# Optimization experiments

Hardware: AMD Instinct MI355X
Metric: run time of the kernel (lower is better)

The kernel has to match this reference:

```python
import jax, jax.numpy as jnp
import numpy as np


def setup_inputs() -> dict:
    key = jax.random.key(0)
    B, D, C, H = 4096, 64, 128, 512
    ks = jax.random.split(key, 6)
    return {
        "q_z_x_params": jax.random.normal(ks[0], (B, C), jnp.float32),
        "eps": jax.random.normal(ks[1], (B, D), jnp.float32),
        "W1": jax.random.normal(ks[2], (D + C, H), jnp.float32) / np.sqrt(D + C).astype(np.float32),
        "b1": jnp.zeros((H,), jnp.float32),
        "W2": jax.random.normal(ks[3], (H, H), jnp.float32) / np.sqrt(H).astype(np.float32),
        "b2": jnp.zeros((H,), jnp.float32),
        "W3": jax.random.normal(ks[4], (H, 2 * D), jnp.float32) / np.sqrt(H).astype(np.float32),
        "b3": jnp.zeros((2 * D,), jnp.float32),
    }


def _made_masks(D, C, H):
    # Standard MADE degrees, natural ordering; context columns fully connected.
    m_in = np.arange(1, D + 1)                      # input degrees 1..D
    m_h = (np.arange(H) % (D - 1)) + 1              # hidden degrees 1..D-1
    M1 = np.concatenate([m_h[None, :] >= m_in[:, None],
                         np.ones((C, H), bool)], axis=0)   # (D+C, H)
    M2 = m_h[None, :] >= m_h[:, None]               # (H, H)
    m_out = np.tile(np.arange(1, D + 1), 2)         # (2D,) mean||prescale
    M3 = m_out[None, :] > m_h[:, None]              # (H, 2D)
    f32 = jnp.float32
    return jnp.asarray(M1, f32), jnp.asarray(M2, f32), jnp.asarray(M3, f32)


def reference(q_z_x_params, eps, W1, b1, W2, b2, W3, b3):
    B, D = eps.shape
    C = q_z_x_params.shape[1]
    H = W2.shape[0]
    M1, M2, M3 = _made_masks(D, C, H)
    mW1, mW2, mW3 = W1 * M1, W2 * M2, W3 * M3

    def made(z):
        x = jnp.concatenate([z, q_z_x_params], axis=1)   # (B, D+C)
        h1 = jax.nn.relu(x @ mW1 + b1)
        h2 = jax.nn.relu(h1 @ mW2 + b2)
        out = h2 @ mW3 + b3                              # (B, 2D)
        return out[:, :D], out[:, D:]

    def step(z, i):
        mean, prescale = made(z)
        mu_i = jnp.take(mean, i, axis=1)                 # (B,)
        scale_i = jax.nn.softplus(jnp.take(prescale, i, axis=1))
        z_i = mu_i + scale_i * jnp.take(eps, i, axis=1)  # reparameterized Normal sample
        z = z.at[:, i].set(z_i)
        return z, None

    z0 = jnp.zeros((B, D), eps.dtype)
    z_sample, _ = jax.lax.scan(step, z0, jnp.arange(D))
    return z_sample
```

## Files before the change

kernel.cpp:

```cpp
#include <hip/hip_runtime.h>
#include <math.h>

#define DD 64
#define CC 128
#define HH 512
#define BATCH 4096

typedef __attribute__((ext_vector_type(2))) float f32x2;
typedef unsigned long long u64;

__device__ __forceinline__ f32x2 splat2(float x) { f32x2 v; v[0] = x; v[1] = x; return v; }

__device__ __forceinline__ f32x2 pk_fma(f32x2 a, f32x2 b, f32x2 c) {
    f32x2 d;
    asm("v_pk_fma_f32 %0, %1, %2, %3" : "=v"(d) : "v"(a), "v"(b), "v"(c));
    return d;
}
__device__ __forceinline__ f32x2 pk_fma_s(u64 hpair, f32x2 b, f32x2 c) {
    f32x2 d;
    asm("v_pk_fma_f32 %0, %1, %2, %3" : "=v"(d) : "s"(hpair), "v"(b), "v"(c));
    return d;
}

__device__ __forceinline__ float fast_softplus(float x) {
    float t = exp2f(-fabsf(x) * 1.44269504f);
    return fmaxf(x, 0.f) + 0.69314718f * log2f(1.f + t);
}

__device__ __forceinline__ float bcast(float x, int l) {
    return __int_as_float(__builtin_amdgcn_readlane(__float_as_int(x), l));
}
__device__ __forceinline__ u64 rl_pair(float x, int l) {
    unsigned u = (unsigned)__builtin_amdgcn_readlane(__float_as_int(x), l);
    return ((u64)u << 32) | u;
}

typedef const __attribute__((address_space(1))) void* as1_cptr;
typedef __attribute__((address_space(3))) void* as3_ptr;
__device__ __forceinline__ void glds16(const float* g, float* l) {
    __builtin_amdgcn_global_load_lds((as1_cptr)g, (as3_ptr)l, 16, 0, 0);
}

__global__ __launch_bounds__(512, 2) void made_sample(
    const float* __restrict__ ctx,
    const float* __restrict__ eps,
    const float* __restrict__ W1,
    const float* __restrict__ b1,
    const float* __restrict__ W2,
    const float* __restrict__ b2,
    const float* __restrict__ W3,
    const float* __restrict__ b3,
    float* __restrict__ out)
{
    const int lane  = threadIdx.x & 63;
    const int w     = threadIdx.x >> 6;
    const int rbase = blockIdx.x * 16 + w * 2;
    const int jbase = 8 * lane;

    __shared__ float sbuf[2][10 * HH];
    __shared__ float w3sb[2][5 * 256];

    int deg[8];
    #pragma unroll
    for (int u = 0; u < 8; ++u) deg[u] = (jbase + u) % 63 + 1;

    auto load8v = [&](const float* base_, f32x2* r_) {
        float4 a = *(const float4*)(base_ + lane * 4);
        float4 b = *(const float4*)(base_ + 256 + lane * 4);
        r_[0][0] = a.x; r_[0][1] = a.y; r_[1][0] = a.z; r_[1][1] = a.w;
        r_[2][0] = b.x; r_[2][1] = b.y; r_[3][0] = b.z; r_[3][1] = b.w;
    };
    auto stage_row = [&](const float* src, float* dst) {
        glds16(src + lane * 8,     dst);
        glds16(src + lane * 8 + 4, dst + 256);
    };
    auto stage_w3pair = [&](int k0, int k1, float* dst) {
        const float* g = (lane < 32) ? (W3 + k0 * (2 * DD) + lane * 4)
                                     : (W3 + k1 * (2 * DD) + (lane - 32) * 4);
        glds16(g, dst);
    };

    f32x2 p1[2][4], p2[2][4], acc[2];
    #pragma unroll
    for (int j = 0; j < 4; ++j) {
        f32x2 t1, t2;
        t1[0] = b1[jbase + 2 * j]; t1[1] = b1[jbase + 2 * j + 1];
        t2[0] = b2[jbase + 2 * j]; t2[1] = b2[jbase + 2 * j + 1];
        p1[0][j] = t1; p1[1][j] = t1;
        p2[0][j] = t2; p2[1][j] = t2;
    }
    acc[0] = splat2(0.f);
    acc[1] = splat2(0.f);

    float ca[2], cb[2], ep[2];
    #pragma unroll
    for (int r = 0; r < 2; ++r) {
        ca[r] = ctx[(rbase + r) * CC + lane];
        cb[r] = ctx[(rbase + r) * CC + 64 + lane];
        ep[r] = eps[(rbase + r) * DD + lane];
    }
    const float b3m = b3[lane];
    const float b3p = b3[64 + lane];

    auto stage_ctx = [&](int ch, float* buf) {
        stage_row(W1 + (DD + 8 * ch + w) * HH, buf + w * HH);
    };
    auto stage_step = [&](int in, float* buf, float* w3buf) {
        if (in == 0) {
            if (w == 1) stage_row(W1, buf + 9 * HH);
            return;
        }
        const int basen = in - 1;
        const bool h9n = basen < 8;
        stage_row(W2 + (basen + 63 * w) * HH, buf + w * HH);
        if (w == 0 && h9n) stage_row(W2 + (basen + 504) * HH, buf + 8 * HH);
        if (w == 1) stage_row(W1 + in * HH, buf + 9 * HH);
        if (w >= 2 && w <= 5) {
            const int p = w - 2;
            stage_w3pair(basen + 63 * (2 * p), basen + 63 * (2 * p + 1),
                         w3buf + p * 256);
        }
        if (w == 6 && h9n)
            stage_w3pair(basen + 504, basen + 504, w3buf + 4 * 256);
    };

    stage_ctx(0, sbuf[0]);
    __syncthreads();
    #pragma unroll 1
    for (int ch = 0; ch < 16; ++ch) {
        float* cur = sbuf[ch & 1];
        if (ch < 15) stage_ctx(ch + 1, sbuf[(ch + 1) & 1]);
        else         stage_step(0, sbuf[0], w3sb[0]);
        f32x2 cw[8][4];
        #pragma unroll
        for (int q = 0; q < 8; ++q) load8v(cur + q * HH, cw[q]);
        __builtin_amdgcn_sched_barrier(0);
        #pragma unroll
        for (int q = 0; q < 8; ++q) {
            const int c = 8 * ch + q;
            #pragma unroll
            for (int r = 0; r < 2; ++r) {
                const u64 cvp = rl_pair((ch < 8) ? ca[r] : cb[r], c & 63);
                #pragma unroll
                for (int j = 0; j < 4; ++j) p1[r][j] = pk_fma_s(cvp, cw[q][j], p1[r][j]);
            }
        }
        __syncthreads();
    }

    float z[2] = {0.f, 0.f};

    #pragma unroll 1
    for (int i = 0; i < DD; ++i) {
        float* cur = sbuf[i & 1];
        const float* w3s = w3sb[i & 1];

        if (i < 63) stage_step(i + 1, sbuf[(i + 1) & 1], w3sb[(i + 1) & 1]);

        f32x2 w1v[4];
        load8v(cur + 9 * HH, w1v);
        f32x2 wv[9][4];
        float wa[9], wb[9];
        if (i > 0) {
            #pragma unroll
            for (int t = 0; t < 9; ++t) load8v(cur + t * HH, wv[t]);
            #pragma unroll
            for (int t = 0; t < 9; ++t) {
                wa[t] = w3s[t * 128 + lane];
                wb[t] = w3s[t * 128 + 64 + lane];
            }
        }
        __builtin_amdgcn_sched_barrier(0);

        if (i > 0) {
            const int base = i - 1;
            const bool h9 = base < 8;

            float m0 = 0.f, m1 = 0.f;
            #pragma unroll
            for (int u = 0; u < 8; ++u) {
                const bool e = (deg[u] == i);
                m0 = e ? p1[0][u >> 1][u & 1] : m0;
                m1 = e ? p1[1][u >> 1][u & 1] : m1;
            }
            m0 = fmaxf(m0, 0.f);
            m1 = fmaxf(m1, 0.f);

            #pragma unroll
            for (int t = 0; t < 8; ++t) {
                const int k = base + 63 * t;
                const u64 h0 = rl_pair(m0, k >> 3);
                const u64 h1 = rl_pair(m1, k >> 3);
                #pragma unroll
                for (int j = 0; j < 4; ++j) {
                    p2[0][j] = pk_fma_s(h0, wv[t][j], p2[0][j]);
                    p2[1][j] = pk_fma_s(h1, wv[t][j], p2[1][j]);
                }
            }
            if (h9) {
                const u64 h0 = rl_pair(m0, 63);
                const u64 h1 = rl_pair(m1, 63);
                #pragma unroll
                for (int j = 0; j < 4; ++j) {
                    p2[0][j] = pk_fma_s(h0, wv[8][j], p2[0][j]);
                    p2[1][j] = pk_fma_s(h1, wv[8][j], p2[1][j]);
                }
            }

            float g0 = 0.f, g1 = 0.f;
            #pragma unroll
            for (int u = 0; u < 8; ++u) {
                const bool e = (deg[u] == i);
                g0 = e ? p2[0][u >> 1][u & 1] : g0;
                g1 = e ? p2[1][u >> 1][u & 1] : g1;
            }
            g0 = fmaxf(g0, 0.f);
            g1 = fmaxf(g1, 0.f);

            #pragma unroll
            for (int t = 0; t < 8; ++t) {
                const int k = base + 63 * t;
                const float h0 = bcast(g0, k >> 3);
                const float h1 = bcast(g1, k >> 3);
                acc[0][0] = fmaf(h0, wa[t], acc[0][0]);
                acc[0][1] = fmaf(h0, wb[t], acc[0][1]);
                acc[1][0] = fmaf(h1, wa[t], acc[1][0]);
                acc[1][1] = fmaf(h1, wb[t], acc[1][1]);
            }
            if (h9) {
                const float h0 = bcast(g0, 63);
                const float h1 = bcast(g1, 63);
                acc[0][0] = fmaf(h0, wa[8], acc[0][0]);
                acc[0][1] = fmaf(h0, wb[8], acc[0][1]);
                acc[1][0] = fmaf(h1, wa[8], acc[1][0]);
                acc[1][1] = fmaf(h1, wb[8], acc[1][1]);
            }
        }

        {
            #pragma unroll
            for (int r = 0; r < 2; ++r) {
                const float am = acc[r][0] + b3m;
                const float ap = acc[r][1] + b3p;
                const float sp = fast_softplus(ap);
                const float zc = fmaf(sp, ep[r], am);
                const float zi = bcast(zc, i);
                if (lane == i) z[r] = zi;
                const u64 zp = rl_pair(zc, i);
                #pragma unroll
                for (int j = 0; j < 4; ++j) p1[r][j] = pk_fma_s(zp, w1v[j], p1[r][j]);
            }
        }

        __syncthreads();
    }

    #pragma unroll
    for (int r = 0; r < 2; ++r) out[(rbase + r) * DD + lane] = z[r];
}

extern "C" void kernel_launch(void* const* d_in, const int* in_sizes, int n_in,
                              void* d_out, int out_size, void* d_ws, size_t ws_size,
                              hipStream_t stream) {
    const float* ctx = (const float*)d_in[0];
    const float* eps = (const float*)d_in[1];
    const float* W1  = (const float*)d_in[2];
    const float* b1  = (const float*)d_in[3];
    const float* W2  = (const float*)d_in[4];
    const float* b2  = (const float*)d_in[5];
    const float* W3  = (const float*)d_in[6];
    const float* b3  = (const float*)d_in[7];
    (void)d_ws; (void)ws_size; (void)in_sizes; (void)n_in; (void)out_size;

    made_sample<<<BATCH / 16, 512, 0, stream>>>(ctx, eps, W1, b1, W2, b2, W3, b3,
                                                (float*)d_out);
}
```

Baseline: 197.4 us.

## Process one row per wave and double the block count for occupancy

Each wave now handles one batch row instead of two, so the grid doubles to 512 blocks and launch bounds request 4 blocks per CU. Register arrays shrink and the bulk LDS prefetch into registers with sched barriers is replaced by per-iteration loads. The aim is more resident waves to hide latency. The cost is that every shared weight row staged into LDS is reused by half as many rows, so global-to-LDS staging traffic and LDS reads per row double. LDS use per block (about 51KB) may also cap how many of the requested 4 blocks actually fit on a CU.

```diff
diff --git a/kernel.cpp b/kernel.cpp
--- a/kernel.cpp
+++ b/kernel.cpp
@@ -11,11 +11,6 @@
 
 __device__ __forceinline__ f32x2 splat2(float x) { f32x2 v; v[0] = x; v[1] = x; return v; }
 
-__device__ __forceinline__ f32x2 pk_fma(f32x2 a, f32x2 b, f32x2 c) {
-    f32x2 d;
-    asm("v_pk_fma_f32 %0, %1, %2, %3" : "=v"(d) : "v"(a), "v"(b), "v"(c));
-    return d;
-}
 __device__ __forceinline__ f32x2 pk_fma_s(u64 hpair, f32x2 b, f32x2 c) {
     f32x2 d;
     asm("v_pk_fma_f32 %0, %1, %2, %3" : "=v"(d) : "s"(hpair), "v"(b), "v"(c));
@@ -41,7 +36,7 @@
     __builtin_amdgcn_global_load_lds((as1_cptr)g, (as3_ptr)l, 16, 0, 0);
 }
 
-__global__ __launch_bounds__(512, 2) void made_sample(
+__global__ __launch_bounds__(512, 4) void made_sample(
     const float* __restrict__ ctx,
     const float* __restrict__ eps,
     const float* __restrict__ W1,
@@ -54,7 +49,7 @@
 {
     const int lane  = threadIdx.x & 63;
     const int w     = threadIdx.x >> 6;
-    const int rbase = blockIdx.x * 16 + w * 2;
+    const int rrow  = blockIdx.x * 8 + w;
     const int jbase = 8 * lane;
 
     __shared__ float sbuf[2][10 * HH];
@@ -80,25 +75,17 @@
         glds16(g, dst);
     };
 
-    f32x2 p1[2][4], p2[2][4], acc[2];
+    f32x2 p1[4], p2[4], acc;
     #pragma unroll
     for (int j = 0; j < 4; ++j) {
-        f32x2 t1, t2;
-        t1[0] = b1[jbase + 2 * j]; t1[1] = b1[jbase + 2 * j + 1];
-        t2[0] = b2[jbase + 2 * j]; t2[1] = b2[jbase + 2 * j + 1];
-        p1[0][j] = t1; p1[1][j] = t1;
-        p2[0][j] = t2; p2[1][j] = t2;
+        p1[j][0] = b1[jbase + 2 * j]; p1[j][1] = b1[jbase + 2 * j + 1];
+        p2[j][0] = b2[jbase + 2 * j]; p2[j][1] = b2[jbase + 2 * j + 1];
     }
-    acc[0] = splat2(0.f);
-    acc[1] = splat2(0.f);
-
-    float ca[2], cb[2], ep[2];
-    #pragma unroll
-    for (int r = 0; r < 2; ++r) {
-        ca[r] = ctx[(rbase + r) * CC + lane];
-        cb[r] = ctx[(rbase + r) * CC + 64 + lane];
-        ep[r] = eps[(rbase + r) * DD + lane];
-    }
+    acc = splat2(0.f);
+
+    const float ca = ctx[rrow * CC + lane];
+    const float cb = ctx[rrow * CC + 64 + lane];
+    const float ep = eps[rrow * DD + lane];
     const float b3m = b3[lane];
     const float b3p = b3[64 + lane];
 
@@ -131,24 +118,19 @@
         float* cur = sbuf[ch & 1];
         if (ch < 15) stage_ctx(ch + 1, sbuf[(ch + 1) & 1]);
         else         stage_step(0, sbuf[0], w3sb[0]);
-        f32x2 cw[8][4];
-        #pragma unroll
-        for (int q = 0; q < 8; ++q) load8v(cur + q * HH, cw[q]);
-        __builtin_amdgcn_sched_barrier(0);
         #pragma unroll
         for (int q = 0; q < 8; ++q) {
+            f32x2 cw[4];
+            load8v(cur + q * HH, cw);
             const int c = 8 * ch + q;
-            #pragma unroll
-            for (int r = 0; r < 2; ++r) {
-                const u64 cvp = rl_pair((ch < 8) ? ca[r] : cb[r], c & 63);
-                #pragma unroll
-                for (int j = 0; j < 4; ++j) p1[r][j] = pk_fma_s(cvp, cw[q][j], p1[r][j]);
-            }
+            const u64 cvp = rl_pair((ch < 8) ? ca : cb, c & 63);
+            #pragma unroll
+            for (int j = 0; j < 4; ++j) p1[j] = pk_fma_s(cvp, cw[j], p1[j]);
         }
         __syncthreads();
     }
 
-    float z[2] = {0.f, 0.f};
+    float z = 0.f;
 
     #pragma unroll 1
     for (int i = 0; i < DD; ++i) {
@@ -159,104 +141,73 @@
 
         f32x2 w1v[4];
         load8v(cur + 9 * HH, w1v);
-        f32x2 wv[9][4];
-        float wa[9], wb[9];
-        if (i > 0) {
-            #pragma unroll
-            for (int t = 0; t < 9; ++t) load8v(cur + t * HH, wv[t]);
-            #pragma unroll
-            for (int t = 0; t < 9; ++t) {
-                wa[t] = w3s[t * 128 + lane];
-                wb[t] = w3s[t * 128 + 64 + lane];
-            }
-        }
-        __builtin_amdgcn_sched_barrier(0);
 
         if (i > 0) {
             const int base = i - 1;
             const bool h9 = base < 8;
 
-            float m0 = 0.f, m1 = 0.f;
-            #pragma unroll
-            for (int u = 0; u < 8; ++u) {
-                const bool e = (deg[u] == i);
-                m0 = e ? p1[0][u >> 1][u & 1] : m0;
-                m1 = e ? p1[1][u >> 1][u & 1] : m1;
-            }
+            float m0 = 0.f;
+            #pragma unroll
+            for (int u = 0; u < 8; ++u)
+                m0 = (deg[u] == i) ? p1[u >> 1][u & 1] : m0;
             m0 = fmaxf(m0, 0.f);
-            m1 = fmaxf(m1, 0.f);
 
             #pragma unroll
             for (int t = 0; t < 8; ++t) {
                 const int k = base + 63 * t;
+                f32x2 wv[4];
+                load8v(cur + t * HH, wv);
                 const u64 h0 = rl_pair(m0, k >> 3);
-                const u64 h1 = rl_pair(m1, k >> 3);
                 #pragma unroll
-                for (int j = 0; j < 4; ++j) {
-                    p2[0][j] = pk_fma_s(h0, wv[t][j], p2[0][j]);
-                    p2[1][j] = pk_fma_s(h1, wv[t][j], p2[1][j]);
-                }
+                for (int j = 0; j < 4; ++j) p2[j] = pk_fma_s(h0, wv[j], p2[j]);
             }
             if (h9) {
+                f32x2 wv[4];
+                load8v(cur + 8 * HH, wv);
                 const u64 h0 = rl_pair(m0, 63);
-                const u64 h1 = rl_pair(m1, 63);
                 #pragma unroll
-                for (int j = 0; j < 4; ++j) {
-                    p2[0][j] = pk_fma_s(h0, wv[8][j], p2[0][j]);
-                    p2[1][j] = pk_fma_s(h1, wv[8][j], p2[1][j]);
-                }
-            }
-
-            float g0 = 0.f, g1 = 0.f;
-            #pragma unroll
-            for (int u = 0; u < 8; ++u) {
-                const bool e = (deg[u] == i);
-                g0 = e ? p2[0][u >> 1][u & 1] : g0;
-                g1 = e ? p2[1][u >> 1][u & 1] : g1;
-            }
+                for (int j = 0; j < 4; ++j) p2[j] = pk_fma_s(h0, wv[j], p2[j]);
+            }
+
+            float g0 = 0.f;
+            #pragma unroll
+            for (int u = 0; u < 8; ++u)
+                g0 = (deg[u] == i) ? p2[u >> 1][u & 1] : g0;
             g0 = fmaxf(g0, 0.f);
-            g1 = fmaxf(g1, 0.f);
 
             #pragma unroll
             for (int t = 0; t < 8; ++t) {
                 const int k = base + 63 * t;
+                const float wa = w3s[t * 128 + lane];
+                const float wb = w3s[t * 128 + 64 + lane];
                 const float h0 = bcast(g0, k >> 3);
-                const float h1 = bcast(g1, k >> 3);
-                acc[0][0] = fmaf(h0, wa[t], acc[0][0]);
-                acc[0][1] = fmaf(h0, wb[t], acc[0][1]);
-                acc[1][0] = fmaf(h1, wa[t], acc[1][0]);
-                acc[1][1] = fmaf(h1, wb[t], acc[1][1]);
+                acc[0] = fmaf(h0, wa, acc[0]);
+                acc[1] = fmaf(h0, wb, acc[1]);
             }
             if (h9) {
+                const float wa = w3s[8 * 128 + lane];
+                const float wb = w3s[8 * 128 + 64 + lane];
                 const float h0 = bcast(g0, 63);
-                const float h1 = bcast(g1, 63);
-                acc[0][0] = fmaf(h0, wa[8], acc[0][0]);
-                acc[0][1] = fmaf(h0, wb[8], acc[0][1]);
-                acc[1][0] = fmaf(h1, wa[8], acc[1][0]);
-                acc[1][1] = fmaf(h1, wb[8], acc[1][1]);
+                acc[0] = fmaf(h0, wa, acc[0]);
+                acc[1] = fmaf(h0, wb, acc[1]);
             }
         }
 
         {
-            #pragma unroll
-            for (int r = 0; r < 2; ++r) {
-                const float am = acc[r][0] + b3m;
-                const float ap = acc[r][1] + b3p;
-                const float sp = fast_softplus(ap);
-                const float zc = fmaf(sp, ep[r], am);
-                const float zi = bcast(zc, i);
-                if (lane == i) z[r] = zi;
-                const u64 zp = rl_pair(zc, i);
-                #pragma unroll
-                for (int j = 0; j < 4; ++j) p1[r][j] = pk_fma_s(zp, w1v[j], p1[r][j]);
-            }
+            const float am = acc[0] + b3m;
+            const float ap = acc[1] + b3p;
+            const float sp = fast_softplus(ap);
+            const float zc = fmaf(sp, ep, am);
+            if (lane == i) z = bcast(zc, i);
+            const u64 zp = rl_pair(zc, i);
+            #pragma unroll
+            for (int j = 0; j < 4; ++j) p1[j] = pk_fma_s(zp, w1v[j], p1[j]);
         }
 
         __syncthreads();
     }
 
-    #pragma unroll
-    for (int r = 0; r < 2; ++r) out[(rbase + r) * DD + lane] = z[r];
+    out[rrow * DD + lane] = z;
 }
 
 extern "C" void kernel_launch(void* const* d_in, const int* in_sizes, int n_in,
@@ -272,6 +223,6 @@
     const float* b3  = (const float*)d_in[7];
     (void)d_ws; (void)ws_size; (void)in_sizes; (void)n_in; (void)out_size;
 
-    made_sample<<<BATCH / 16, 512, 0, stream>>>(ctx, eps, W1, b1, W2, b2, W3, b3,
-                                                (float*)d_out);
-}
+    made_sample<<<BATCH / 8, 512, 0, stream>>>(ctx, eps, W1, b1, W2, b2, W3, b3,
+                                               (float*)d_out);
+}
```

New measurement: 175.0 us (median of 2 runs). 1.13x faster.

## Halve block size to four waves, use inline-asm LDS reads and packed W3 FMAs

Applied to the files above, without the earlier changes.

Shrinks each block from 8 to 4 wavefronts (8 rows per block, twice as many blocks), so each wave now stages two W2 rows and W3 pairs per step. Weight reads from LDS switch to explicit ds_read_b128/ds_read2_b32 inline asm followed by a single waitcnt. The W3 output accumulation becomes packed FMAs split across two accumulator chains, and the degree selects become a sum tree. Doubling the block count doubles the total weight staging traffic into LDS, in exchange for less barrier contention per block and more blocks to overlap with each other.

```diff
diff --git a/kernel.cpp b/kernel.cpp
--- a/kernel.cpp
+++ b/kernel.cpp
@@ -10,12 +10,9 @@
 typedef unsigned long long u64;
 
 __device__ __forceinline__ f32x2 splat2(float x) { f32x2 v; v[0] = x; v[1] = x; return v; }
-
-__device__ __forceinline__ f32x2 pk_fma(f32x2 a, f32x2 b, f32x2 c) {
-    f32x2 d;
-    asm("v_pk_fma_f32 %0, %1, %2, %3" : "=v"(d) : "v"(a), "v"(b), "v"(c));
-    return d;
-}
+__device__ __forceinline__ f32x2 lo2(float4 v) { f32x2 r; r[0] = v.x; r[1] = v.y; return r; }
+__device__ __forceinline__ f32x2 hi2(float4 v) { f32x2 r; r[0] = v.z; r[1] = v.w; return r; }
+
 __device__ __forceinline__ f32x2 pk_fma_s(u64 hpair, f32x2 b, f32x2 c) {
     f32x2 d;
     asm("v_pk_fma_f32 %0, %1, %2, %3" : "=v"(d) : "s"(hpair), "v"(b), "v"(c));
@@ -37,11 +34,23 @@
 
 typedef const __attribute__((address_space(1))) void* as1_cptr;
 typedef __attribute__((address_space(3))) void* as3_ptr;
+typedef const __attribute__((address_space(3))) float* as3c;
 __device__ __forceinline__ void glds16(const float* g, float* l) {
     __builtin_amdgcn_global_load_lds((as1_cptr)g, (as3_ptr)l, 16, 0, 0);
 }
 
-__global__ __launch_bounds__(512, 2) void made_sample(
+__device__ __forceinline__ float4 ldsb128(const float* p) {
+    float4 r;
+    asm volatile("ds_read_b128 %0, %1" : "=v"(r) : "v"((as3c)p));
+    return r;
+}
+__device__ __forceinline__ f32x2 ldsr2(const float* p) {
+    f32x2 r;
+    asm volatile("ds_read2_b32 %0, %1 offset0:0 offset1:64" : "=v"(r) : "v"((as3c)p));
+    return r;
+}
+
+__global__ __launch_bounds__(256, 2) void made_sample(
     const float* __restrict__ ctx,
     const float* __restrict__ eps,
     const float* __restrict__ W1,
@@ -54,7 +63,7 @@
 {
     const int lane  = threadIdx.x & 63;
     const int w     = threadIdx.x >> 6;
-    const int rbase = blockIdx.x * 16 + w * 2;
+    const int rbase = blockIdx.x * 8 + w * 2;
     const int jbase = 8 * lane;
 
     __shared__ float sbuf[2][10 * HH];
@@ -64,12 +73,6 @@
     #pragma unroll
     for (int u = 0; u < 8; ++u) deg[u] = (jbase + u) % 63 + 1;
 
-    auto load8v = [&](const float* base_, f32x2* r_) {
-        float4 a = *(const float4*)(base_ + lane * 4);
-        float4 b = *(const float4*)(base_ + 256 + lane * 4);
-        r_[0][0] = a.x; r_[0][1] = a.y; r_[1][0] = a.z; r_[1][1] = a.w;
-        r_[2][0] = b.x; r_[2][1] = b.y; r_[3][0] = b.z; r_[3][1] = b.w;
-    };
     auto stage_row = [&](const float* src, float* dst) {
         glds16(src + lane * 8,     dst);
         glds16(src + lane * 8 + 4, dst + 256);
@@ -80,7 +83,7 @@
         glds16(g, dst);
     };
 
-    f32x2 p1[2][4], p2[2][4], acc[2];
+    f32x2 p1[2][4], p2[2][4];
     #pragma unroll
     for (int j = 0; j < 4; ++j) {
         f32x2 t1, t2;
@@ -89,8 +92,9 @@
         p1[0][j] = t1; p1[1][j] = t1;
         p2[0][j] = t2; p2[1][j] = t2;
     }
-    acc[0] = splat2(0.f);
-    acc[1] = splat2(0.f);
+    f32x2 accA[2], accB[2];
+    accA[0] = splat2(0.f); accA[1] = splat2(0.f);
+    accB[0] = splat2(0.f); accB[1] = splat2(0.f);
 
     float ca[2], cb[2], ep[2];
     #pragma unroll
@@ -103,7 +107,8 @@
     const float b3p = b3[64 + lane];
 
     auto stage_ctx = [&](int ch, float* buf) {
-        stage_row(W1 + (DD + 8 * ch + w) * HH, buf + w * HH);
+        stage_row(W1 + (DD + 8 * ch + 2 * w) * HH,     buf + (2 * w) * HH);
+        stage_row(W1 + (DD + 8 * ch + 2 * w + 1) * HH, buf + (2 * w + 1) * HH);
     };
     auto stage_step = [&](int in, float* buf, float* w3buf) {
         if (in == 0) {
@@ -112,15 +117,13 @@
         }
         const int basen = in - 1;
         const bool h9n = basen < 8;
-        stage_row(W2 + (basen + 63 * w) * HH, buf + w * HH);
+        stage_row(W2 + (basen + 63 * w) * HH,       buf + w * HH);
+        stage_row(W2 + (basen + 63 * (4 + w)) * HH, buf + (4 + w) * HH);
         if (w == 0 && h9n) stage_row(W2 + (basen + 504) * HH, buf + 8 * HH);
         if (w == 1) stage_row(W1 + in * HH, buf + 9 * HH);
-        if (w >= 2 && w <= 5) {
-            const int p = w - 2;
-            stage_w3pair(basen + 63 * (2 * p), basen + 63 * (2 * p + 1),
-                         w3buf + p * 256);
-        }
-        if (w == 6 && h9n)
+        stage_w3pair(basen + 63 * (2 * w), basen + 63 * (2 * w + 1),
+                     w3buf + w * 256);
+        if (w == 2 && h9n)
             stage_w3pair(basen + 504, basen + 504, w3buf + 4 * 256);
     };
 
@@ -131,9 +134,14 @@
         float* cur = sbuf[ch & 1];
         if (ch < 15) stage_ctx(ch + 1, sbuf[(ch + 1) & 1]);
         else         stage_step(0, sbuf[0], w3sb[0]);
-        f32x2 cw[8][4];
+        const float* lb = cur + lane * 4;
+        float4 cwL[8], cwH[8];
         #pragma unroll
-        for (int q = 0; q < 8; ++q) load8v(cur + q * HH, cw[q]);
+        for (int q = 0; q < 8; ++q) {
+            cwL[q] = ldsb128(lb + q * HH);
+            cwH[q] = ldsb128(lb + q * HH + 256);
+        }
+        asm volatile("s_waitcnt lgkmcnt(0)" ::: "memory");
         __builtin_amdgcn_sched_barrier(0);
         #pragma unroll
         for (int q = 0; q < 8; ++q) {
@@ -141,8 +149,10 @@
             #pragma unroll
             for (int r = 0; r < 2; ++r) {
                 const u64 cvp = rl_pair((ch < 8) ? ca[r] : cb[r], c & 63);
-                #pragma unroll
-                for (int j = 0; j < 4; ++j) p1[r][j] = pk_fma_s(cvp, cw[q][j], p1[r][j]);
+                p1[r][0] = pk_fma_s(cvp, lo2(cwL[q]), p1[r][0]);
+                p1[r][1] = pk_fma_s(cvp, hi2(cwL[q]), p1[r][1]);
+                p1[r][2] = pk_fma_s(cvp, lo2(cwH[q]), p1[r][2]);
+                p1[r][3] = pk_fma_s(cvp, hi2(cwH[q]), p1[r][3]);
             }
         }
         __syncthreads();
@@ -157,98 +167,114 @@
 
         if (i < 63) stage_step(i + 1, sbuf[(i + 1) & 1], w3sb[(i + 1) & 1]);
 
-        f32x2 w1v[4];
-        load8v(cur + 9 * HH, w1v);
-        f32x2 wv[9][4];
-        float wa[9], wb[9];
+        const float* lb = cur + lane * 4;
+        float4 wL[9], wH[9];
+        f32x2 w3v[9];
         if (i > 0) {
             #pragma unroll
-            for (int t = 0; t < 9; ++t) load8v(cur + t * HH, wv[t]);
-            #pragma unroll
             for (int t = 0; t < 9; ++t) {
-                wa[t] = w3s[t * 128 + lane];
-                wb[t] = w3s[t * 128 + 64 + lane];
-            }
-        }
+                wL[t] = ldsb128(lb + t * HH);
+                wH[t] = ldsb128(lb + t * HH + 256);
+            }
+            #pragma unroll
+            for (int t = 0; t < 9; ++t) w3v[t] = ldsr2(w3s + t * 128 + lane);
+        }
+        const float4 w1L = ldsb128(lb + 9 * HH);
+        const float4 w1H = ldsb128(lb + 9 * HH + 256);
+        asm volatile("s_waitcnt lgkmcnt(0)" ::: "memory");
         __builtin_amdgcn_sched_barrier(0);
 
         if (i > 0) {
             const int base = i - 1;
             const bool h9 = base < 8;
 
-            float m0 = 0.f, m1 = 0.f;
-            #pragma unroll
-            for (int u = 0; u < 8; ++u) {
-                const bool e = (deg[u] == i);
-                m0 = e ? p1[0][u >> 1][u & 1] : m0;
-                m1 = e ? p1[1][u >> 1][u & 1] : m1;
-            }
-            m0 = fmaxf(m0, 0.f);
-            m1 = fmaxf(m1, 0.f);
+            float m[2];
+            #pragma unroll
+            for (int r = 0; r < 2; ++r) {
+                float s[8];
+                #pragma unroll
+                for (int u = 0; u < 8; ++u)
+                    s[u] = (deg[u] == i) ? p1[r][u >> 1][u & 1] : 0.f;
+                const float sv = ((s[0] + s[1]) + (s[2] + s[3]))
+                               + ((s[4] + s[5]) + (s[6] + s[7]));
+                m[r] = fmaxf(sv, 0.f);
+            }
 
             #pragma unroll
             for (int t = 0; t < 8; ++t) {
                 const int k = base + 63 * t;
-                const u64 h0 = rl_pair(m0, k >> 3);
-                const u64 h1 = rl_pair(m1, k >> 3);
+                const u64 h0 = rl_pair(m[0], k >> 3);
+                const u64 h1 = rl_pair(m[1], k >> 3);
+                p2[0][0] = pk_fma_s(h0, lo2(wL[t]), p2[0][0]);
+                p2[0][1] = pk_fma_s(h0, hi2(wL[t]), p2[0][1]);
+                p2[0][2] = pk_fma_s(h0, lo2(wH[t]), p2[0][2]);
+                p2[0][3] = pk_fma_s(h0, hi2(wH[t]), p2[0][3]);
+                p2[1][0] = pk_fma_s(h1, lo2(wL[t]), p2[1][0]);
+                p2[1][1] = pk_fma_s(h1, hi2(wL[t]), p2[1][1]);
+                p2[1][2] = pk_fma_s(h1, lo2(wH[t]), p2[1][2]);
+                p2[1][3] = pk_fma_s(h1, hi2(wH[t]), p2[1][3]);
+            }
+            if (h9) {
+                const u64 h0 = rl_pair(m[0], 63);
+                const u64 h1 = rl_pair(m[1], 63);
+                p2[0][0] = pk_fma_s(h0, lo2(wL[8]), p2[0][0]);
+                p2[0][1] = pk_fma_s(h0, hi2(wL[8]), p2[0][1]);
+                p2[0][2] = pk_fma_s(h0, lo2(wH[8]), p2[0][2]);
+                p2[0][3] = pk_fma_s(h0, hi2(wH[8]), p2[0][3]);
+                p2[1][0] = pk_fma_s(h1, lo2(wL[8]), p2[1][0]);
+                p2[1][1] = pk_fma_s(h1, hi2(wL[8]), p2[1][1]);
+                p2[1][2] = pk_fma_s(h1, lo2(wH[8]), p2[1][2]);
+                p2[1][3] = pk_fma_s(h1, hi2(wH[8]), p2[1][3]);
+            }
+
+            float g[2];
+            #pragma unroll
+            for (int r = 0; r < 2; ++r) {
+                float s[8];
                 #pragma unroll
-                for (int j = 0; j < 4; ++j) {
-                    p2[0][j] = pk_fma_s(h0, wv[t][j], p2[0][j]);
-                    p2[1][j] = pk_fma_s(h1, wv[t][j], p2[1][j]);
-                }
-            }
-            if (h9) {
-                const u64 h0 = rl_pair(m0, 63);
-                const u64 h1 = rl_pair(m1, 63);
-                #pragma unroll
-                for (int j = 0; j < 4; ++j) {
-                    p2[0][j] = pk_fma_s(h0, wv[8][j], p2[0][j]);
-                    p2[1][j] = pk_fma_s(h1, wv[8][j], p2[1][j]);
-                }
-            }
-
-            float g0 = 0.f, g1 = 0.f;
-            #pragma unroll
-            for (int u = 0; u < 8; ++u) {
-                const bool e = (deg[u] == i);
-                g0 = e ? p2[0][u >> 1][u & 1] : g0;
-                g1 = e ? p2[1][u >> 1][u & 1] : g1;
-            }
-            g0 = fmaxf(g0, 0.f);
-            g1 = fmaxf(g1, 0.f);
+                for (int u = 0; u < 8; ++u)
+                    s[u] = (deg[u] == i) ? p2[r][u >> 1][u & 1] : 0.f;
+                const float sv = ((s[0] + s[1]) + (s[2] + s[3]))
+                               + ((s[4] + s[5]) + (s[6] + s[7]));
+                g[r] = fmaxf(sv, 0.f);
+            }
 
             #pragma unroll
             for (int t = 0; t < 8; ++t) {
                 const int k = base + 63 * t;
-                const float h0 = bcast(g0, k >> 3);
-                const float h1 = bcast(g1, k >> 3);
-                acc[0][0] = fmaf(h0, wa[t], acc[0][0]);
-                acc[0][1] = fmaf(h0, wb[t], acc[0][1]);
-                acc[1][0] = fmaf(h1, wa[t], acc[1][0]);
-                acc[1][1] = fmaf(h1, wb[t], acc[1][1]);
+                const u64 h0 = rl_pair(g[0], k >> 3);
+                const u64 h1 = rl_pair(g[1], k >> 3);
+                if (t & 1) {
+                    accB[0] = pk_fma_s(h0, w3v[t], accB[0]);
+                    accB[1] = pk_fma_s(h1, w3v[t], accB[1]);
+                } else {
+                    accA[0] = pk_fma_s(h0, w3v[t], accA[0]);
+                    accA[1] = pk_fma_s(h1, w3v[t], accA[1]);
+                }
             }
             if (h9) {
-                const float h0 = bcast(g0, 63);
-                const float h1 = bcast(g1, 63);
-                acc[0][0] = fmaf(h0, wa[8], acc[0][0]);
-                acc[0][1] = fmaf(h0, wb[8], acc[0][1]);
-                acc[1][0] = fmaf(h1, wa[8], acc[1][0]);
-                acc[1][1] = fmaf(h1, wb[8], acc[1][1]);
+                const u64 h0 = rl_pair(g[0], 63);
+                const u64 h1 = rl_pair(g[1], 63);
+                accB[0] = pk_fma_s(h0, w3v[8], accB[0]);
+                accB[1] = pk_fma_s(h1, w3v[8], accB[1]);
             }
         }
 
         {
             #pragma unroll
             for (int r = 0; r < 2; ++r) {
-                const float am = acc[r][0] + b3m;
-                const float ap = acc[r][1] + b3p;
+                const f32x2 at = accA[r] + accB[r];
+                const float am = at[0] + b3m;
+                const float ap = at[1] + b3p;
                 const float sp = fast_softplus(ap);
                 const float zc = fmaf(sp, ep[r], am);
                 const float zi = bcast(zc, i);
                 if (lane == i) z[r] = zi;
                 const u64 zp = rl_pair(zc, i);
-                #pragma unroll
-                for (int j = 0; j < 4; ++j) p1[r][j] = pk_fma_s(zp, w1v[j], p1[r][j]);
+                p1[r][0] = pk_fma_s(zp, lo2(w1L), p1[r][0]);
+                p1[r][1] = pk_fma_s(zp, hi2(w1L), p1[r][1]);
+                p1[r][2] = pk_fma_s(zp, lo2(w1H), p1[r][2]);
+                p1[r][3] = pk_fma_s(zp, hi2(w1H), p1[r][3]);
             }
         }
 
@@ -272,6 +298,6 @@
     const float* b3  = (const float*)d_in[7];
     (void)d_ws; (void)ws_size; (void)in_sizes; (void)n_in; (void)out_size;
 
-    made_sample<<<BATCH / 16, 512, 0, stream>>>(ctx, eps, W1, b1, W2, b2, W3, b3,
-                                                (float*)d_out);
-}
+    made_sample<<<BATCH / 8, 256, 0, stream>>>(ctx, eps, W1, b1, W2, b2, W3, b3,
+                                               (float*)d_out);
+}
```

Measured after the change: 189.5 us. 4.0% less time.
